# Kernel tuning notes

Hardware: AMD Instinct MI355X
Metric: run time of the kernel (lower is better)

## Reference

```python
import jax, jax.numpy as jnp
import numpy as np

BLOCK_LEN = 64

def _segsum(x):
    # x: (..., T) -> (..., T, T) with entry [t, s] = sum_{u=s+1..t} x[u], -inf above diagonal
    T = x.shape[-1]
    cs = jnp.cumsum(x, axis=-1)
    ss = cs[..., :, None] - cs[..., None, :]
    mask = jnp.tril(jnp.ones((T, T), dtype=bool))
    return jnp.where(mask, ss, -jnp.inf)

def setup_inputs() -> dict:
    key = jax.random.key(0)
    kx, ka, kb, kc = jax.random.split(key, 4)
    b, L, h, p, n = 4, 4096, 32, 64, 16
    X = jax.random.normal(kx, (b, L, h, p), dtype=jnp.float32)
    # negative, small-magnitude A so exp(cumsum(A)) stays finite (decaying SSM),
    # matching the math of the module while keeping the baseline numerically sane
    A = -0.1 * jnp.abs(jax.random.normal(ka, (b, L, h), dtype=jnp.float32))
    B = jax.random.normal(kb, (b, L, h, n), dtype=jnp.float32)
    C = jax.random.normal(kc, (b, L, h, n), dtype=jnp.float32)
    return {"X": X, "A": A, "B": B, "C": C}

def reference(X, A, B, C):
    b, L, h, p = X.shape
    n = B.shape[-1]
    l = BLOCK_LEN
    c = L // l
    # chunk into blocks
    Xb = X.reshape(b, c, l, h, p)                       # b c l h p
    Ab = A.reshape(b, c, l, h).transpose(0, 3, 1, 2)    # b h c l
    Bb = B.reshape(b, c, l, h, n)                       # b c l h n
    Cb = C.reshape(b, c, l, h, n)                       # b c l h n
    A_cumsum = jnp.cumsum(Ab, axis=-1)                  # b h c l
    # intra-chunk (diagonal) term; equals the fused per-timestep scan
    # h_t = exp(A_t)*h_{t-1} + B_t*x_t ; y_t = C_t . h_t
    Lmat = jnp.exp(_segsum(Ab))                         # b h c l l (lower-tri)
    Y_diag = jnp.einsum('bclhn,bcshn,bhcls,bcshp->bclhp', Cb, Bb, Lmat, Xb)
    # per-chunk end states
    decay_states = jnp.exp(A_cumsum[..., -1:] - A_cumsum)  # b h c l
    states = jnp.einsum('bclhn,bhcl,bclhp->bchpn', Bb, decay_states, Xb)
    states = jnp.concatenate([jnp.zeros_like(states[:, :1]), states], axis=1)  # b (c+1) h p n
    # inter-chunk recurrence via segment-sum of chunk totals
    decay_chunk = jnp.exp(_segsum(jnp.pad(A_cumsum[..., -1], ((0, 0), (0, 0), (1, 0)))))  # b h (c+1) (c+1)
    new_states = jnp.einsum('bhzc,bchpn->bzhpn', decay_chunk, states)
    states = new_states[:, :-1]                          # b c h p n
    # state -> output contribution
    state_decay_out = jnp.exp(A_cumsum)                  # b h c l
    Y_off = jnp.einsum('bclhn,bchpn,bhcl->bclhp', Cb, states, state_decay_out)
    return (Y_diag + Y_off).reshape(b, L, h, p)
```

## Files before the change

kernel.cpp:

```cpp
#include <hip/hip_runtime.h>

#define BATCH   4
#define SEQLEN  4096
#define NHEADS  32
#define PDIM    64
#define NDIM    16
#define CHUNK   64
#define NCHUNK  64

typedef short v8s __attribute__((ext_vector_type(8)));
typedef float v4f __attribute__((ext_vector_type(4)));

__device__ __forceinline__ short f2bf(float f) {
    union { float f; unsigned u; } x; x.f = f;
    unsigned r = (x.u + 0x7FFFu + ((x.u >> 16) & 1u)) >> 16;
    return (short)r;
}
__device__ __forceinline__ float bf2f(short s) {
    union { unsigned u; float f; } x; x.u = ((unsigned)(unsigned short)s) << 16;
    return x.f;
}

__global__ __launch_bounds__(256) void k_states(
    const float* __restrict__ X, const float* __restrict__ A,
    const float* __restrict__ Bm, float* __restrict__ states,
    float* __restrict__ csum)
{
    const int cc = blockIdx.x, hh = blockIdx.y, bb = blockIdx.z;
    const int tid = threadIdx.x;
    __shared__ float sX[CHUNK][PDIM];
    __shared__ float sB[CHUNK][NDIM];
    __shared__ float sA[CHUNK];
    __shared__ float sCum[CHUNK];
    __shared__ float sDec[CHUNK];
    const int t0 = bb * SEQLEN + cc * CHUNK;

    if (tid < CHUNK) sA[tid] = A[(t0 + tid) * NHEADS + hh];
    for (int e = tid; e < CHUNK * PDIM; e += 256) {
        int t = e >> 6, pp = e & 63;
        sX[t][pp] = X[((size_t)(t0 + t) * NHEADS + hh) * PDIM + pp];
    }
    for (int e = tid; e < CHUNK * NDIM; e += 256) {
        int t = e >> 4, nn = e & 15;
        sB[t][nn] = Bm[((size_t)(t0 + t) * NHEADS + hh) * NDIM + nn];
    }
    __syncthreads();
    if (tid < CHUNK) {
        float s = 0.f;
        for (int j = 0; j <= tid; ++j) s += sA[j];
        sCum[tid] = s;
    }
    __syncthreads();
    const float ctot = sCum[CHUNK - 1];
    if (tid < CHUNK) sDec[tid] = __expf(ctot - sCum[tid]);
    __syncthreads();

    const int pp = tid & 63, ng = tid >> 6;
    float4 acc = make_float4(0.f, 0.f, 0.f, 0.f);
    for (int t = 0; t < CHUNK; ++t) {
        float x = sX[t][pp] * sDec[t];
        float4 b4 = *(const float4*)&sB[t][ng * 4];
        acc.x += x * b4.x; acc.y += x * b4.y;
        acc.z += x * b4.z; acc.w += x * b4.w;
    }
    float* sp = states + ((size_t)(bb * NHEADS + hh) * NCHUNK + cc) * (PDIM * NDIM)
                       + pp * NDIM + ng * 4;
    *(float4*)sp = acc;
    if (tid == 0) csum[(bb * NHEADS + hh) * NCHUNK + cc] = ctot;
}

__global__ __launch_bounds__(256) void k_scan(
    float* __restrict__ states, const float* __restrict__ csum)
{
    const int bh = blockIdx.y;
    const int q  = blockIdx.x;
    const int el = q * 256 + threadIdx.x;
    __shared__ float sE[NCHUNK];
    if (threadIdx.x < NCHUNK) sE[threadIdx.x] = __expf(csum[bh * NCHUNK + threadIdx.x]);
    __syncthreads();
    float S = 0.f;
    float* base = states + (size_t)bh * NCHUNK * (PDIM * NDIM) + el;
    for (int z = 0; z < NCHUNK; ++z) {
        float v = base[z * (PDIM * NDIM)];
        base[z * (PDIM * NDIM)] = S;
        S = sE[z] * S + v;
    }
}

__global__ __launch_bounds__(256) void k_out(
    const float* __restrict__ X, const float* __restrict__ A,
    const float* __restrict__ Bm, const float* __restrict__ Cm,
    const float* __restrict__ states, float* __restrict__ Y)
{
    const int cc = blockIdx.x, hh = blockIdx.y, bb = blockIdx.z;
    const int tid = threadIdx.x;
    const int lane = tid & 63, W = tid >> 6;
    const int qq = lane >> 4, nn = lane & 15;
    const int t0 = bb * SEQLEN + cc * CHUNK;

    __shared__ __align__(16) char uBuf[CHUNK * (PDIM + 1) * 4];
    float (*sXraw)[PDIM + 1] = (float (*)[PDIM + 1])uBuf;
    short* gF = (short*)uBuf;
    __shared__ __align__(16) short xF[4096];
    __shared__ __align__(16) short cF[2048];
    __shared__ __align__(16) short bF[2048];
    __shared__ __align__(16) short sF[2048];
    __shared__ float sA[CHUNK];
    __shared__ float sCum[CHUNK];

    if (tid < CHUNK) sA[tid] = A[(t0 + tid) * NHEADS + hh];
    {
        const int sb = tid >> 4, p4 = (tid & 15) * 4;
        for (int i = 0; i < 4; ++i) {
            int s = sb + i * 16;
            const float4 v = *(const float4*)&X[((size_t)(t0 + s) * NHEADS + hh) * PDIM + p4];
            sXraw[s][p4]     = v.x; sXraw[s][p4 + 1] = v.y;
            sXraw[s][p4 + 2] = v.z; sXraw[s][p4 + 3] = v.w;
        }
    }
    {
        const int r = tid >> 2, nn0 = (tid & 3) * 4;
        const int off = ((r >> 4) * 64 + (nn0 >> 3) * 16 + (r & 15)) * 8 + (nn0 & 7);
        float4 cv = *(const float4*)&Cm[((size_t)(t0 + r) * NHEADS + hh) * NDIM + nn0];
        cF[off] = f2bf(cv.x); cF[off + 1] = f2bf(cv.y);
        cF[off + 2] = f2bf(cv.z); cF[off + 3] = f2bf(cv.w);
        float4 bv = *(const float4*)&Bm[((size_t)(t0 + r) * NHEADS + hh) * NDIM + nn0];
        bF[off] = f2bf(bv.x); bF[off + 1] = f2bf(bv.y);
        bF[off + 2] = f2bf(bv.z); bF[off + 3] = f2bf(bv.w);
        const float* sp = states + ((size_t)(bb * NHEADS + hh) * NCHUNK + cc) * (PDIM * NDIM)
                                 + r * NDIM + nn0;
        float4 sv = *(const float4*)sp;
        sF[off] = f2bf(sv.x); sF[off + 1] = f2bf(sv.y);
        sF[off + 2] = f2bf(sv.z); sF[off + 3] = f2bf(sv.w);
    }
    {
        const v8s z8 = {0, 0, 0, 0, 0, 0, 0, 0};
        for (int z = tid; z < 384; z += 256) {
            short* base = (z < 128) ? cF : (z < 256) ? bF : sF;
            int idx = z & 127;
            int off = (idx >> 5) * 512 + 256 + (idx & 31) * 8;
            *(v8s*)&base[off] = z8;
        }
    }
    __syncthreads();

    if (tid < CHUNK) {
        float s = 0.f;
        for (int j = 0; j <= tid; ++j) s += sA[j];
        sCum[tid] = s;
    }
    for (int c = tid; c < 512; c += 256) {
        int cn = c & 15, cq = (c >> 4) & 3, nt = (c >> 6) & 3, kk = c >> 8;
        int srow = kk * 32 + cq * 8, p = nt * 16 + cn;
        v8s v;
        for (int j = 0; j < 8; ++j) v[j] = f2bf(sXraw[srow + j][p]);
        *(v8s*)&xF[c * 8] = v;
    }
    __syncthreads();

    const v8s cfrag = *(const v8s*)&cF[(W * 64 + lane) * 8];
    const v4f zero = {0.f, 0.f, 0.f, 0.f};
    for (int st = 0; st < 4; ++st) {
        const int kk = st >> 1, q2 = (st & 1) * 2 + (nn >> 3), j2 = nn & 7;
        if (st <= W) {
            v8s bfrag = *(const v8s*)&bF[(st * 64 + lane) * 8];
            v4f acc = __builtin_amdgcn_mfma_f32_16x16x32_bf16(cfrag, bfrag, zero, 0, 0, 0);
            const int s = st * 16 + nn;
            const float cums = sCum[s];
            for (int r = 0; r < 4; ++r) {
                int t = W * 16 + qq * 4 + r;
                float g = (t >= s) ? acc[r] * __expf(sCum[t] - cums) : 0.f;
                gF[((W * 2 + kk) * 64 + q2 * 16 + qq * 4 + r) * 8 + j2] = f2bf(g);
            }
        } else if (kk == 0 || W >= 2) {
            for (int r = 0; r < 4; ++r)
                gF[((W * 2 + kk) * 64 + q2 * 16 + qq * 4 + r) * 8 + j2] = 0;
        }
    }
    const float et = __expf(sCum[W * 16 + nn]);
    v8s cefrag;
    for (int j = 0; j < 8; ++j) cefrag[j] = f2bf(bf2f(cfrag[j]) * et);
    __syncthreads();

    const v8s ga0 = *(const v8s*)&gF[((W * 2 + 0) * 64 + lane) * 8];
    const bool usekk1 = (W >= 2);
    v8s ga1 = {0, 0, 0, 0, 0, 0, 0, 0};
    if (usekk1) ga1 = *(const v8s*)&gF[((W * 2 + 1) * 64 + lane) * 8];
    v4f acc[4];
    for (int nt = 0; nt < 4; ++nt) {
        v8s sfrag = *(const v8s*)&sF[(nt * 64 + lane) * 8];
        v4f a = __builtin_amdgcn_mfma_f32_16x16x32_bf16(cefrag, sfrag, zero, 0, 0, 0);
        v8s x0 = *(const v8s*)&xF[((0 * 4 + nt) * 64 + lane) * 8];
        a = __builtin_amdgcn_mfma_f32_16x16x32_bf16(ga0, x0, a, 0, 0, 0);
        if (usekk1) {
            v8s x1 = *(const v8s*)&xF[((1 * 4 + nt) * 64 + lane) * 8];
            a = __builtin_amdgcn_mfma_f32_16x16x32_bf16(ga1, x1, a, 0, 0, 0);
        }
        acc[nt] = a;
    }
    for (int r = 0; r < 4; ++r) {
        int t = W * 16 + qq * 4 + r;
        float* yp = Y + ((size_t)(t0 + t) * NHEADS + hh) * PDIM + nn;
        for (int nt = 0; nt < 4; ++nt) yp[nt * 16] = acc[nt][r];
    }
}

extern "C" void kernel_launch(void* const* d_in, const int* in_sizes, int n_in,
                              void* d_out, int out_size, void* d_ws, size_t ws_size,
                              hipStream_t stream) {
    const float* X  = (const float*)d_in[0];
    const float* A  = (const float*)d_in[1];
    const float* Bm = (const float*)d_in[2];
    const float* Cm = (const float*)d_in[3];
    float* Y = (float*)d_out;

    float* states = (float*)d_ws;
    float* csum   = states + (size_t)BATCH * NHEADS * NCHUNK * PDIM * NDIM;

    dim3 grid(NCHUNK, NHEADS, BATCH);
    k_states<<<grid, 256, 0, stream>>>(X, A, Bm, states, csum);
    dim3 gscan(4, BATCH * NHEADS, 1);
    k_scan<<<gscan, 256, 0, stream>>>(states, csum);
    k_out<<<grid, 256, 0, stream>>>(X, A, Bm, Cm, states, Y);
}
```

Baseline: 373.1 us.

## Compute chunk states with bf16 MFMA and batch loads in state scan

The per-chunk state computation moves from a scalar FMA loop to bf16 MFMA. X is loaded with float4 reads, scaled by the decay factors and packed into fragment layouts in shared memory. The inter-chunk scan now loads all 64 chunk values into registers before the recurrence and writes them back afterwards, so memory loads no longer serialize with the dependent chain. Costs are bf16 rounding of the states and higher register pressure in the scan kernel.

```diff
diff --git a/kernel.cpp b/kernel.cpp
--- a/kernel.cpp
+++ b/kernel.cpp
@@ -28,21 +28,35 @@
 {
     const int cc = blockIdx.x, hh = blockIdx.y, bb = blockIdx.z;
     const int tid = threadIdx.x;
-    __shared__ float sX[CHUNK][PDIM];
-    __shared__ float sB[CHUNK][NDIM];
+    const int lane = tid & 63, W = tid >> 6;
+    const int t0 = bb * SEQLEN + cc * CHUNK;
+
+    __shared__ __align__(16) float sXraw[CHUNK][PDIM + 1];
+    __shared__ __align__(16) short aF[4096];
+    __shared__ __align__(16) short bF[1024];
     __shared__ float sA[CHUNK];
     __shared__ float sCum[CHUNK];
     __shared__ float sDec[CHUNK];
-    const int t0 = bb * SEQLEN + cc * CHUNK;
 
     if (tid < CHUNK) sA[tid] = A[(t0 + tid) * NHEADS + hh];
-    for (int e = tid; e < CHUNK * PDIM; e += 256) {
-        int t = e >> 6, pp = e & 63;
-        sX[t][pp] = X[((size_t)(t0 + t) * NHEADS + hh) * PDIM + pp];
-    }
-    for (int e = tid; e < CHUNK * NDIM; e += 256) {
-        int t = e >> 4, nn = e & 15;
-        sB[t][nn] = Bm[((size_t)(t0 + t) * NHEADS + hh) * NDIM + nn];
+    {
+        const int sb = tid >> 4, p4 = (tid & 15) * 4;
+        for (int i = 0; i < 4; ++i) {
+            int s = sb + i * 16;
+            const float4 v = *(const float4*)&X[((size_t)(t0 + s) * NHEADS + hh) * PDIM + p4];
+            sXraw[s][p4]     = v.x; sXraw[s][p4 + 1] = v.y;
+            sXraw[s][p4 + 2] = v.z; sXraw[s][p4 + 3] = v.w;
+        }
+    }
+    {
+        const int r = tid >> 2, n0 = (tid & 3) * 4;
+        float4 bv = *(const float4*)&Bm[((size_t)(t0 + r) * NHEADS + hh) * NDIM + n0];
+        const int kk = r >> 5, q = (r >> 3) & 3, j = r & 7;
+        const int base = (kk * 64 + q * 16) * 8 + j;
+        bF[base + (n0 + 0) * 8] = f2bf(bv.x);
+        bF[base + (n0 + 1) * 8] = f2bf(bv.y);
+        bF[base + (n0 + 2) * 8] = f2bf(bv.z);
+        bF[base + (n0 + 3) * 8] = f2bf(bv.w);
     }
     __syncthreads();
     if (tid < CHUNK) {
@@ -51,40 +65,54 @@
         sCum[tid] = s;
     }
     __syncthreads();
-    const float ctot = sCum[CHUNK - 1];
-    if (tid < CHUNK) sDec[tid] = __expf(ctot - sCum[tid]);
-    __syncthreads();
-
-    const int pp = tid & 63, ng = tid >> 6;
-    float4 acc = make_float4(0.f, 0.f, 0.f, 0.f);
-    for (int t = 0; t < CHUNK; ++t) {
-        float x = sX[t][pp] * sDec[t];
-        float4 b4 = *(const float4*)&sB[t][ng * 4];
-        acc.x += x * b4.x; acc.y += x * b4.y;
-        acc.z += x * b4.z; acc.w += x * b4.w;
-    }
-    float* sp = states + ((size_t)(bb * NHEADS + hh) * NCHUNK + cc) * (PDIM * NDIM)
-                       + pp * NDIM + ng * 4;
-    *(float4*)sp = acc;
-    if (tid == 0) csum[(bb * NHEADS + hh) * NCHUNK + cc] = ctot;
+    if (tid < CHUNK) sDec[tid] = __expf(sCum[CHUNK - 1] - sCum[tid]);
+    __syncthreads();
+
+    for (int c = tid; c < 512; c += 256) {
+        const int m = c & 15, q = (c >> 4) & 3, pt = (c >> 6) & 3, kk = c >> 8;
+        const int srow = kk * 32 + q * 8, p = pt * 16 + m;
+        v8s v;
+        for (int j = 0; j < 8; ++j) v[j] = f2bf(sXraw[srow + j][p] * sDec[srow + j]);
+        *(v8s*)&aF[((pt * 2 + kk) * 64 + q * 16 + m) * 8] = v;
+    }
+    __syncthreads();
+
+    const v4f zero = {0.f, 0.f, 0.f, 0.f};
+    v8s a0 = *(const v8s*)&aF[((W * 2 + 0) * 64 + lane) * 8];
+    v8s a1 = *(const v8s*)&aF[((W * 2 + 1) * 64 + lane) * 8];
+    v8s b0 = *(const v8s*)&bF[(0 * 64 + lane) * 8];
+    v8s b1 = *(const v8s*)&bF[(1 * 64 + lane) * 8];
+    v4f acc = __builtin_amdgcn_mfma_f32_16x16x32_bf16(a0, b0, zero, 0, 0, 0);
+    acc = __builtin_amdgcn_mfma_f32_16x16x32_bf16(a1, b1, acc, 0, 0, 0);
+
+    const int q = lane >> 4, n = lane & 15;
+    float* sp = states + ((size_t)(bb * NHEADS + hh) * NCHUNK + cc) * (PDIM * NDIM);
+    for (int r = 0; r < 4; ++r)
+        sp[(W * 16 + q * 4 + r) * NDIM + n] = acc[r];
+    if (tid == 0) csum[(bb * NHEADS + hh) * NCHUNK + cc] = sCum[CHUNK - 1];
 }
 
 __global__ __launch_bounds__(256) void k_scan(
     float* __restrict__ states, const float* __restrict__ csum)
 {
     const int bh = blockIdx.y;
-    const int q  = blockIdx.x;
-    const int el = q * 256 + threadIdx.x;
+    const int el = blockIdx.x * 256 + threadIdx.x;
     __shared__ float sE[NCHUNK];
     if (threadIdx.x < NCHUNK) sE[threadIdx.x] = __expf(csum[bh * NCHUNK + threadIdx.x]);
     __syncthreads();
+    float* base = states + (size_t)bh * NCHUNK * (PDIM * NDIM) + el;
+    float v[NCHUNK];
+#pragma unroll
+    for (int z = 0; z < NCHUNK; ++z) v[z] = base[z * (PDIM * NDIM)];
     float S = 0.f;
-    float* base = states + (size_t)bh * NCHUNK * (PDIM * NDIM) + el;
+#pragma unroll
     for (int z = 0; z < NCHUNK; ++z) {
-        float v = base[z * (PDIM * NDIM)];
-        base[z * (PDIM * NDIM)] = S;
-        S = sE[z] * S + v;
-    }
+        const float nv = v[z];
+        v[z] = S;
+        S = sE[z] * S + nv;
+    }
+#pragma unroll
+    for (int z = 0; z < NCHUNK; ++z) base[z * (PDIM * NDIM)] = v[z];
 }
 
 __global__ __launch_bounds__(256) void k_out(
```

Result: faster. 334.7 us (-10.3%).
